# Performance work log

Measured on AMD Instinct MI355X. Metric: run time of the kernel, lower is better.

Reference implementation:

```python
import jax, jax.numpy as jnp
import numpy as np

EMBED = 256
HEADS = 8
HEAD_DIM = EMBED // HEADS  # 32, even for RoPE
INIT_VAL = 1.0
HEADS_RANGE = 3.0


def rotate_every_two(x):
    # (x1, x2) -> (-x2, x1) on interleaved pairs of last dim
    x1 = x[..., ::2]
    x2 = x[..., 1::2]
    return jnp.stack([-x2, x1], axis=-1).reshape(x.shape)


def theta_shift(x, sin, cos):
    # x: [B, heads, H, W, D]; sin/cos: [H, W, D] broadcast over B, heads
    return x * cos + rotate_every_two(x) * sin


def rel_pos_2d(H, W):
    # RetNetRelPos2d: RoPE angles + per-head exponential decay mask
    angle = 1.0 / (10000.0 ** jnp.linspace(0.0, 1.0, HEAD_DIM // 2))
    angle = jnp.repeat(angle, 2)  # [D]
    idx = jnp.arange(H * W, dtype=jnp.float32)
    sin = jnp.sin(idx[:, None] * angle[None, :]).reshape(H, W, HEAD_DIM)
    cos = jnp.cos(idx[:, None] * angle[None, :]).reshape(H, W, HEAD_DIM)
    h_idx = jnp.arange(HEADS, dtype=jnp.float32)
    decay = jnp.log(1.0 - 2.0 ** (-INIT_VAL - HEADS_RANGE * h_idx / HEADS))  # [heads]
    gh, gw = jnp.meshgrid(jnp.arange(H), jnp.arange(W), indexing='ij')
    grid = jnp.stack([gh, gw], axis=-1).reshape(H * W, 2)  # [N,2]
    dist = jnp.abs(grid[:, None, :] - grid[None, :, :]).sum(-1)  # [N,N] L1 distance
    mask = dist[None, :, :].astype(jnp.float32) * decay[:, None, None]  # [heads,N,N]
    return sin, cos, mask


def setup_inputs() -> dict:
    key = jax.random.key(0)
    ks = jax.random.split(key, 8)
    B, H, W, C = 2, 48, 48, EMBED
    s = 0.02
    return {
        'x': jax.random.normal(ks[0], (B, H, W, C), jnp.float32),
        'Wq': jax.random.normal(ks[1], (C, C), jnp.float32) * s,
        'bq': jnp.zeros((C,), jnp.float32),
        'Wk': jax.random.normal(ks[2], (C, C), jnp.float32) * s,
        'bk': jnp.zeros((C,), jnp.float32),
        'Wv': jax.random.normal(ks[3], (C, C), jnp.float32) * s,
        'bv': jnp.zeros((C,), jnp.float32),
        'lepe_w': jax.random.normal(ks[4], (C, 1, 5, 5), jnp.float32) * s,  # depthwise 5x5
        'lepe_b': jnp.zeros((C,), jnp.float32),
        'Wo': jax.random.normal(ks[5], (C, C), jnp.float32) * s,
        'bo': jnp.zeros((C,), jnp.float32),
    }


def reference(x, Wq, bq, Wk, bk, Wv, bv, lepe_w, lepe_b, Wo, bo):
    B, H, W, C = x.shape
    N = H * W
    sin, cos, mask = rel_pos_2d(H, W)
    scaling = HEAD_DIM ** -0.5

    q = x @ Wq + bq
    k = (x @ Wk + bk) * scaling
    v = x @ Wv + bv

    # lepe: depthwise 5x5 conv on v (BHWC)
    lepe = jax.lax.conv_general_dilated(
        v.transpose(0, 3, 1, 2), lepe_w, (1, 1), 'SAME',
        feature_group_count=C, dimension_numbers=('NCHW', 'OIHW', 'NCHW'))
    lepe = lepe.transpose(0, 2, 3, 1) + lepe_b  # [B,H,W,C]

    def split_heads(t):
        return t.reshape(B, H, W, HEADS, HEAD_DIM).transpose(0, 3, 1, 2, 4)

    qr = theta_shift(split_heads(q), sin, cos).reshape(B, HEADS, N, HEAD_DIM)
    kr = theta_shift(split_heads(k), sin, cos).reshape(B, HEADS, N, HEAD_DIM)
    vv = split_heads(v).reshape(B, HEADS, N, HEAD_DIM)

    attn = jnp.einsum('bhnd,bhmd->bhnm', qr, kr) + mask[None]  # [B,heads,N,N]
    attn = jax.nn.softmax(attn, axis=-1)
    out = jnp.einsum('bhnm,bhmd->bhnd', attn, vv)
    out = out.transpose(0, 2, 1, 3).reshape(B, H, W, C)
    out = out + lepe
    return out @ Wo + bo
```

## Files before the change

kernel.cpp:

```cpp
#include <hip/hip_runtime.h>
#include <hip/hip_bf16.h>
#include <math.h>

#define NN 2304
#define ROWSZ 4608
#define SZ (ROWSZ*256)

typedef __attribute__((ext_vector_type(8))) short short8;
typedef __attribute__((ext_vector_type(4))) float f32x4;

__device__ __forceinline__ float bf2f(unsigned short u) {
    return __uint_as_float(((unsigned int)u) << 16);
}
__device__ __forceinline__ unsigned short f2bf(float f) {
    unsigned int u = __float_as_uint(f);
    u += 0x7FFFu + ((u >> 16) & 1u);
    return (unsigned short)(u >> 16);
}
__device__ __forceinline__ unsigned int pack_bf2(float a, float b) {
    return (unsigned int)f2bf(a) | ((unsigned int)f2bf(b) << 16);
}

template<int F32>
__device__ __forceinline__ float ldin(const void* p, int i) {
    if constexpr (F32) return ((const float*)p)[i];
    else return bf2f(((const unsigned short*)p)[i]);
}

__global__ void detect_kernel(const unsigned int* __restrict__ x, int* __restrict__ flag) {
    int t = threadIdx.x;
    int cnt = 0;
    for (int i = t; i < 256; i += 64) {
        unsigned int e = (x[i] >> 7) & 0xFFu;
        cnt += (e < 87u || e > 167u) ? 1 : 0;
    }
    #pragma unroll
    for (int o = 32; o; o >>= 1) cnt += __shfl_down(cnt, o);
    if (t == 0) *flag = (cnt >= 32) ? 1 : 0;
}

template<int F32>
__device__ __forceinline__ void qkv_body(
    const void* __restrict__ x,
    const void* __restrict__ Wq, const void* __restrict__ bq,
    const void* __restrict__ Wk, const void* __restrict__ bk,
    const void* __restrict__ Wv, const void* __restrict__ bv,
    unsigned short* __restrict__ q, unsigned short* __restrict__ k,
    unsigned short* __restrict__ v, unsigned short* __restrict__ vT,
    float* __restrict__ xs)
{
    const int t = threadIdx.x;
    const int by = blockIdx.y;
    const int row0 = blockIdx.x * 16;
    #pragma unroll
    for (int pass = 0; pass < 2; ++pass) {
        int e = pass*2048 + t*8;
        if constexpr (F32) {
            const float* xp = (const float*)x + row0*256 + e;
            float4 a0 = *reinterpret_cast<const float4*>(xp);
            float4 a1 = *reinterpret_cast<const float4*>(xp + 4);
            *reinterpret_cast<float4*>(&xs[e])   = a0;
            *reinterpret_cast<float4*>(&xs[e+4]) = a1;
        } else {
            const unsigned short* xp = (const unsigned short*)x + row0*256 + e;
            uint4 raw = *reinterpret_cast<const uint4*>(xp);
            const unsigned short* us = reinterpret_cast<const unsigned short*>(&raw);
            #pragma unroll
            for (int j = 0; j < 8; ++j) xs[e + j] = bf2f(us[j]);
        }
    }
    __syncthreads();
    const void* Wsel = (by == 0) ? Wq : (by == 1) ? Wk : Wv;
    const void* bsel = (by == 0) ? bq : (by == 1) ? bk : bv;
    float a[16];
    const float bv0 = ldin<F32>(bsel, t);
    #pragma unroll
    for (int r = 0; r < 16; ++r) a[r] = bv0;
    for (int i0 = 0; i0 < 256; i0 += 4) {
        float w0 = ldin<F32>(Wsel, (i0+0)*256 + t);
        float w1 = ldin<F32>(Wsel, (i0+1)*256 + t);
        float w2 = ldin<F32>(Wsel, (i0+2)*256 + t);
        float w3 = ldin<F32>(Wsel, (i0+3)*256 + t);
        #pragma unroll
        for (int r = 0; r < 16; ++r) {
            float4 xv = *reinterpret_cast<const float4*>(&xs[r*256 + i0]);
            a[r] = fmaf(xv.w,w3, fmaf(xv.z,w2, fmaf(xv.y,w1, fmaf(xv.x,w0, a[r]))));
        }
    }
    if (by == 2) {
        const int b = (row0 >= NN) ? 1 : 0;
        const int n0 = row0 - b*NN;
        const int h = t >> 5, d = t & 31;
        unsigned int vp[8];
        #pragma unroll
        for (int r = 0; r < 16; ++r) v[(row0 + r)*256 + t] = f2bf(a[r]);
        #pragma unroll
        for (int r = 0; r < 8; ++r) vp[r] = pack_bf2(a[2*r], a[2*r+1]);
        unsigned short* vt = vT + ((size_t)(b*8 + h)*32 + d)*NN + n0;
        *reinterpret_cast<uint4*>(vt)     = make_uint4(vp[0], vp[1], vp[2], vp[3]);
        *reinterpret_cast<uint4*>(vt + 8) = make_uint4(vp[4], vp[5], vp[6], vp[7]);
    } else {
        const float scaling = 0.17677669529663687f;
        const int j = (t & 31) >> 1;
        const float ang = exp2f((float)j * (-0.8858474919699633f));
        const bool odd = t & 1;
        unsigned short* dst = (by == 0) ? q : k;
        const float mul = (by == 0) ? 1.0f : scaling;
        #pragma unroll
        for (int r = 0; r < 16; ++r) {
            int bn = row0 + r;
            int n = bn >= NN ? bn - NN : bn;
            float sv, cv;
            sincosf((float)n * ang, &sv, &cv);
            float ap = __shfl_xor(a[r], 1);
            float val = odd ? fmaf(a[r], cv, ap*sv) : fmaf(a[r], cv, -ap*sv);
            dst[bn*256 + t] = f2bf(val * mul);
        }
    }
}

__global__ __launch_bounds__(256) void qkv_kernel(
    const void* __restrict__ x,
    const void* __restrict__ Wq, const void* __restrict__ bq,
    const void* __restrict__ Wk, const void* __restrict__ bk,
    const void* __restrict__ Wv, const void* __restrict__ bv,
    const int* __restrict__ flag,
    unsigned short* __restrict__ q, unsigned short* __restrict__ k,
    unsigned short* __restrict__ v, unsigned short* __restrict__ vT)
{
    __shared__ float xs[16*256];
    if (*flag) qkv_body<1>(x, Wq, bq, Wk, bk, Wv, bv, q, k, v, vT, xs);
    else       qkv_body<0>(x, Wq, bq, Wk, bk, Wv, bv, q, k, v, vT, xs);
}

template<int F32>
__device__ __forceinline__ void lepe_body(const unsigned short* __restrict__ v,
    const void* __restrict__ w, const void* __restrict__ wb,
    unsigned short* __restrict__ lepe)
{
    int c = threadIdx.x;
    int pos = blockIdx.x;
    int b  = pos >= NN ? 1 : 0;
    int yx = pos - b*NN;
    int y  = (yx*21846) >> 20;
    int xx = yx - y*48;
    float acc = ldin<F32>(wb, c);
    #pragma unroll
    for (int ky = 0; ky < 5; ++ky) {
        int yy = y + ky - 2;
        if ((unsigned)yy >= 48u) continue;
        #pragma unroll
        for (int kx = 0; kx < 5; ++kx) {
            int xc = xx + kx - 2;
            if ((unsigned)xc >= 48u) continue;
            acc = fmaf(bf2f(v[((b*NN + yy*48 + xc)<<8) + c]), ldin<F32>(w, c*25 + ky*5 + kx), acc);
        }
    }
    lepe[(pos<<8) + c] = f2bf(acc);
}

__global__ __launch_bounds__(256) void lepe_kernel(const unsigned short* __restrict__ v,
    const void* __restrict__ w, const void* __restrict__ wb,
    const int* __restrict__ flag, unsigned short* __restrict__ lepe)
{
    if (*flag) lepe_body<1>(v, w, wb, lepe);
    else       lepe_body<0>(v, w, wb, lepe);
}

template<int DIRECT>
__global__ __launch_bounds__(256) void attn_kernel(
    const unsigned short* __restrict__ q, const unsigned short* __restrict__ k,
    const unsigned short* __restrict__ vT, unsigned short* __restrict__ o,
    float* __restrict__ pacc, float* __restrict__ pl)
{
    __shared__ char smem[17920];
    char* KsB = smem;
    char* VtB = smem + 5120;
    const int t = threadIdx.x;
    const int w = t >> 6, lane = t & 63;
    const int q16 = lane & 15, quad = lane >> 4;
    char* PsB = smem + 9728 + w*2048;
    const int bh = blockIdx.y, b = bh >> 3, h = bh & 7;
    const int q0 = blockIdx.x*64 + w*16;
    const int nq = q0 + q16;
    const int yq = (nq*21846) >> 20, xq = nq - yq*48;
    const float decay = logf(1.0f - exp2f(-1.0f - 0.375f*(float)h));
    short8 qfrag = *reinterpret_cast<const short8*>(q + ((size_t)(b*NN + nq))*256 + h*32 + quad*8);
    f32x4 acc0 = {0.f,0.f,0.f,0.f}, acc1 = {0.f,0.f,0.f,0.f};
    const f32x4 zero = {0.f,0.f,0.f,0.f};
    float lacc = 0.0f;
    const unsigned short* kbase = k + (size_t)(b*NN)*256 + h*32;
    const unsigned short* vtb = vT + (size_t)bh*32*NN;
    const int skr = t >> 2, skp = t & 3;
    const int svd = t >> 3, svp = t & 7;
    const int psW = q16*16 + (quad & 1)*8;
    const int qsh = quad >> 1;
    const int nchunk = 36 / gridDim.z;
    const int kt0 = blockIdx.z * nchunk;
    for (int kc = 0; kc < nchunk; ++kc) {
        const int kt = kt0 + kc;
        __syncthreads();
        {
            uint4 kraw = *reinterpret_cast<const uint4*>(kbase + (kt*64 + skr)*256 + skp*8);
            uint4 vraw = *reinterpret_cast<const uint4*>(vtb + svd*NN + kt*64 + svp*8);
            *reinterpret_cast<uint4*>(KsB + skr*80 + skp*16) = kraw;
            *reinterpret_cast<uint4*>(VtB + svd*144 + svp*16) = vraw;
        }
        __syncthreads();
        f32x4 st[4];
        #pragma unroll
        for (int tt = 0; tt < 4; ++tt) {
            short8 kf = *reinterpret_cast<const short8*>(KsB + (tt*16 + q16)*80 + quad*16);
            st[tt] = __builtin_amdgcn_mfma_f32_16x16x32_bf16(kf, qfrag, zero, 0, 0, 0);
        }
        unsigned int pk[8];
        float lsum = 0.0f;
        #pragma unroll
        for (int tt = 0; tt < 4; ++tt) {
            float p[4];
            #pragma unroll
            for (int r = 0; r < 4; ++r) {
                int kpos = kt*64 + tt*16 + quad*4 + r;
                int yk = (kpos*21846) >> 20;
                int xk = kpos - yk*48;
                int dist = __usad((unsigned)yq, (unsigned)yk, __usad((unsigned)xq, (unsigned)xk, 0u));
                p[r] = __expf(fmaf(decay, (float)dist, st[tt][r]));
                lsum += p[r];
            }
            pk[tt*2]   = __builtin_amdgcn_perm(__float_as_uint(p[1]), __float_as_uint(p[0]), 0x07060302);
            pk[tt*2+1] = __builtin_amdgcn_perm(__float_as_uint(p[3]), __float_as_uint(p[2]), 0x07060302);
        }
        lacc += lsum;
        #pragma unroll
        for (int tt = 0; tt < 4; ++tt) {
            uint2 pp; pp.x = pk[tt*2]; pp.y = pk[tt*2+1];
            *reinterpret_cast<uint2*>(PsB + (tt >> 1)*1024 + (((tt*2) + qsh) & 3)*256 + psW) = pp;
        }
        #pragma unroll
        for (int kh = 0; kh < 2; ++kh) {
            short8 pf = *reinterpret_cast<const short8*>(PsB + kh*1024 + lane*16);
            short8 v0 = *reinterpret_cast<const short8*>(VtB + q16*144 + kh*64 + quad*16);
            short8 v1 = *reinterpret_cast<const short8*>(VtB + (16 + q16)*144 + kh*64 + quad*16);
            acc0 = __builtin_amdgcn_mfma_f32_16x16x32_bf16(v0, pf, acc0, 0, 0, 0);
            acc1 = __builtin_amdgcn_mfma_f32_16x16x32_bf16(v1, pf, acc1, 0, 0, 0);
        }
    }
    lacc += __shfl_xor(lacc, 16);
    lacc += __shfl_xor(lacc, 32);
    if constexpr (DIRECT) {
        float invl = 1.0f / lacc;
        unsigned short* orow = o + ((size_t)(b*NN + nq))*256 + h*32;
        uint2 w0, w1;
        w0.x = pack_bf2(acc0[0]*invl, acc0[1]*invl);
        w0.y = pack_bf2(acc0[2]*invl, acc0[3]*invl);
        w1.x = pack_bf2(acc1[0]*invl, acc1[1]*invl);
        w1.y = pack_bf2(acc1[2]*invl, acc1[3]*invl);
        *reinterpret_cast<uint2*>(orow + quad*4)      = w0;
        *reinterpret_cast<uint2*>(orow + 16 + quad*4) = w1;
    } else {
        float* pb = pacc + ((size_t)(blockIdx.z*16 + bh)*NN + nq)*32;
        *reinterpret_cast<f32x4*>(pb + quad*4)      = acc0;
        *reinterpret_cast<f32x4*>(pb + 16 + quad*4) = acc1;
        if (quad == 0) pl[((size_t)blockIdx.z*16 + bh)*NN + nq] = lacc;
    }
}

template<int F32>
__device__ __forceinline__ void out_body(
    const unsigned short* __restrict__ o,
    const float* __restrict__ pacc, const float* __restrict__ pl,
    const unsigned short* __restrict__ lp,
    const void* __restrict__ Wo, const void* __restrict__ bo,
    void* __restrict__ out, float* __restrict__ as, int nsplit)
{
    const int t = threadIdx.x;
    const int row0 = blockIdx.x * 8;
    {
        const int e = t*8;
        const int r = t >> 5;
        const int nqr = row0 + r;
        const int ch = e & 255;
        uint4 ub = *reinterpret_cast<const uint4*>(lp + nqr*256 + ch);
        const unsigned short* bu = reinterpret_cast<const unsigned short*>(&ub);
        if (nsplit == 0) {
            uint4 ua = *reinterpret_cast<const uint4*>(o + nqr*256 + ch);
            const unsigned short* au = reinterpret_cast<const unsigned short*>(&ua);
            #pragma unroll
            for (int jj = 0; jj < 8; ++jj) as[e+jj] = bf2f(au[jj]) + bf2f(bu[jj]);
        } else {
            const int b = nqr >= NN ? 1 : 0;
            const int nq = nqr - b*NN;
            const int h = ch >> 5, d = ch & 31;
            const int bh = b*8 + h;
            float s[8] = {0.f,0.f,0.f,0.f,0.f,0.f,0.f,0.f};
            float lsum = 0.0f;
            for (int p = 0; p < nsplit; ++p) {
                const float* pb = pacc + ((size_t)(p*16 + bh)*NN + nq)*32 + d;
                f32x4 v0 = *reinterpret_cast<const f32x4*>(pb);
                f32x4 v1 = *reinterpret_cast<const f32x4*>(pb + 4);
                #pragma unroll
                for (int jj = 0; jj < 4; ++jj) { s[jj] += v0[jj]; s[4+jj] += v1[jj]; }
                lsum += pl[((size_t)p*16 + bh)*NN + nq];
            }
            float invl = 1.0f / lsum;
            #pragma unroll
            for (int jj = 0; jj < 8; ++jj) as[e+jj] = fmaf(s[jj], invl, bf2f(bu[jj]));
        }
    }
    __syncthreads();
    float a[8];
    const float bv = ldin<F32>(bo, t);
    #pragma unroll
    for (int r = 0; r < 8; ++r) a[r] = bv;
    for (int i0 = 0; i0 < 256; i0 += 4) {
        float w0 = ldin<F32>(Wo, (i0+0)*256 + t);
        float w1 = ldin<F32>(Wo, (i0+1)*256 + t);
        float w2 = ldin<F32>(Wo, (i0+2)*256 + t);
        float w3 = ldin<F32>(Wo, (i0+3)*256 + t);
        #pragma unroll
        for (int r = 0; r < 8; ++r) {
            float4 xv = *reinterpret_cast<const float4*>(&as[r*256 + i0]);
            a[r] = fmaf(xv.w,w3, fmaf(xv.z,w2, fmaf(xv.y,w1, fmaf(xv.x,w0, a[r]))));
        }
    }
    #pragma unroll
    for (int r = 0; r < 8; ++r) {
        int idx = (row0+r)*256 + t;
        if constexpr (F32) ((float*)out)[idx] = a[r];
        else ((unsigned short*)out)[idx] = f2bf(a[r]);
    }
}

__global__ __launch_bounds__(256) void out_kernel(
    const unsigned short* __restrict__ o,
    const float* __restrict__ pacc, const float* __restrict__ pl,
    const unsigned short* __restrict__ lp,
    const void* __restrict__ Wo, const void* __restrict__ bo,
    const int* __restrict__ flag, void* __restrict__ out, int nsplit)
{
    __shared__ float as[8*256];
    if (*flag) out_body<1>(o, pacc, pl, lp, Wo, bo, out, as, nsplit);
    else       out_body<0>(o, pacc, pl, lp, Wo, bo, out, as, nsplit);
}

extern "C" void kernel_launch(void* const* d_in, const int* in_sizes, int n_in,
                              void* d_out, int out_size, void* d_ws, size_t ws_size,
                              hipStream_t stream)
{
    const void* x  = d_in[0];
    const void* Wq = d_in[1];
    const void* bq = d_in[2];
    const void* Wk = d_in[3];
    const void* bk = d_in[4];
    const void* Wv = d_in[5];
    const void* bv = d_in[6];
    const void* lw = d_in[7];
    const void* lb = d_in[8];
    const void* Wo = d_in[9];
    const void* bo = d_in[10];

    int* flag = (int*)d_ws;
    unsigned short* qb   = (unsigned short*)((char*)d_ws + 256);
    unsigned short* kbuf = qb   + (size_t)SZ;
    unsigned short* vbuf = kbuf + (size_t)SZ;
    unsigned short* obuf = vbuf + (size_t)SZ;
    unsigned short* lbuf = obuf + (size_t)SZ;
    unsigned short* vtb  = lbuf + (size_t)SZ;

    const size_t base = 256 + 6*(size_t)SZ*2;
    const size_t per_split = (size_t)16*NN*32*4 + (size_t)16*NN*4;
    int nsplit = 0;
    if      (ws_size >= base + 4*per_split) nsplit = 4;
    else if (ws_size >= base + 2*per_split) nsplit = 2;
    else if (ws_size >= base + 1*per_split) nsplit = 1;
    float* pacc = (float*)((char*)d_ws + base);
    float* pl   = pacc + (size_t)(nsplit ? nsplit : 1)*16*NN*32;

    detect_kernel<<<1, 64, 0, stream>>>((const unsigned int*)x, flag);
    qkv_kernel<<<dim3(288,3), 256, 0, stream>>>(x, Wq, bq, Wk, bk, Wv, bv, flag, qb, kbuf, vbuf, vtb);
    lepe_kernel<<<4608, 256, 0, stream>>>(vbuf, lw, lb, flag, lbuf);
    if (nsplit) {
        attn_kernel<0><<<dim3(36, 16, nsplit), 256, 0, stream>>>(qb, kbuf, vtb, obuf, pacc, pl);
    } else {
        attn_kernel<1><<<dim3(36, 16, 1), 256, 0, stream>>>(qb, kbuf, vtb, obuf, pacc, pl);
    }
    out_kernel<<<576, 256, 0, stream>>>(obuf, pacc, pl, lbuf, Wo, bo, flag, d_out, nsplit);
}
```

Measured before the change: 232.8 us.

## Precompute L1 distance table in bytes and use exp2 with log2e folded into K

Adds a kernel that precomputes the 2304x2304 L1 grid-distance table as bytes, which the attention kernel loads instead of recomputing coordinates and distances per score. K is now pre-scaled by log2e and the decay is taken in log2, so the softmax exponent becomes a bare exp2 with no extra multiply. This cuts integer ALU work in the attention inner loop but adds a 5.3 MB table that is written every call and read per query row, plus one more kernel launch.

```diff
diff --git a/kernel.cpp b/kernel.cpp
--- a/kernel.cpp
+++ b/kernel.cpp
@@ -19,6 +19,23 @@
 }
 __device__ __forceinline__ unsigned int pack_bf2(float a, float b) {
     return (unsigned int)f2bf(a) | ((unsigned int)f2bf(b) << 16);
+}
+
+__device__ __forceinline__ float ub2f(unsigned int v, int r) {
+#if defined(__has_builtin)
+#if __has_builtin(__builtin_amdgcn_cvt_f32_ubyte0)
+    switch (r) {
+        case 0: return __builtin_amdgcn_cvt_f32_ubyte0(v);
+        case 1: return __builtin_amdgcn_cvt_f32_ubyte1(v);
+        case 2: return __builtin_amdgcn_cvt_f32_ubyte2(v);
+        default: return __builtin_amdgcn_cvt_f32_ubyte3(v);
+    }
+#else
+    return (float)((v >> (8*r)) & 0xFFu);
+#endif
+#else
+    return (float)((v >> (8*r)) & 0xFFu);
+#endif
 }
 
 template<int F32>
@@ -37,6 +54,26 @@
     #pragma unroll
     for (int o = 32; o; o >>= 1) cnt += __shfl_down(cnt, o);
     if (t == 0) *flag = (cnt >= 32) ? 1 : 0;
+}
+
+__global__ __launch_bounds__(256) void dist_kernel(unsigned char* __restrict__ D) {
+    const int nq = blockIdx.x;
+    const int yq = (nq*21846) >> 20, xq = nq - yq*48;
+    unsigned int* drow = reinterpret_cast<unsigned int*>(D + (size_t)nq*NN);
+    for (int idx = threadIdx.x; idx < 576; idx += 256) {
+        const int kp0 = idx*4;
+        unsigned int wv = 0;
+        #pragma unroll
+        for (int r = 0; r < 4; ++r) {
+            int kp = kp0 + r;
+            int yk = (kp*21846) >> 20;
+            int xk = kp - yk*48;
+            unsigned int dist = __usad((unsigned)yq, (unsigned)yk,
+                                __usad((unsigned)xq, (unsigned)xk, 0u));
+            wv |= dist << (8*r);
+        }
+        drow[idx] = wv;
+    }
 }
 
 template<int F32>
@@ -101,11 +138,12 @@
         *reinterpret_cast<uint4*>(vt + 8) = make_uint4(vp[4], vp[5], vp[6], vp[7]);
     } else {
         const float scaling = 0.17677669529663687f;
+        const float log2e   = 1.4426950408889634f;
         const int j = (t & 31) >> 1;
         const float ang = exp2f((float)j * (-0.8858474919699633f));
         const bool odd = t & 1;
         unsigned short* dst = (by == 0) ? q : k;
-        const float mul = (by == 0) ? 1.0f : scaling;
+        const float mul = (by == 0) ? 1.0f : scaling * log2e;
         #pragma unroll
         for (int r = 0; r < 16; ++r) {
             int bn = row0 + r;
@@ -170,8 +208,8 @@
 template<int DIRECT>
 __global__ __launch_bounds__(256) void attn_kernel(
     const unsigned short* __restrict__ q, const unsigned short* __restrict__ k,
-    const unsigned short* __restrict__ vT, unsigned short* __restrict__ o,
-    float* __restrict__ pacc, float* __restrict__ pl)
+    const unsigned short* __restrict__ vT, const unsigned char* __restrict__ D,
+    unsigned short* __restrict__ o, float* __restrict__ pacc, float* __restrict__ pl)
 {
     __shared__ char smem[17920];
     char* KsB = smem;
@@ -183,14 +221,14 @@
     const int bh = blockIdx.y, b = bh >> 3, h = bh & 7;
     const int q0 = blockIdx.x*64 + w*16;
     const int nq = q0 + q16;
-    const int yq = (nq*21846) >> 20, xq = nq - yq*48;
-    const float decay = logf(1.0f - exp2f(-1.0f - 0.375f*(float)h));
+    const float decay2 = log2f(1.0f - exp2f(-1.0f - 0.375f*(float)h));
     short8 qfrag = *reinterpret_cast<const short8*>(q + ((size_t)(b*NN + nq))*256 + h*32 + quad*8);
     f32x4 acc0 = {0.f,0.f,0.f,0.f}, acc1 = {0.f,0.f,0.f,0.f};
     const f32x4 zero = {0.f,0.f,0.f,0.f};
     float lacc = 0.0f;
     const unsigned short* kbase = k + (size_t)(b*NN)*256 + h*32;
     const unsigned short* vtb = vT + (size_t)bh*32*NN;
+    const unsigned char* Dbase = D + (size_t)nq*NN + quad*4;
     const int skr = t >> 2, skp = t & 3;
     const int svd = t >> 3, svp = t & 7;
     const int psW = q16*16 + (quad & 1)*8;
@@ -199,6 +237,10 @@
     const int kt0 = blockIdx.z * nchunk;
     for (int kc = 0; kc < nchunk; ++kc) {
         const int kt = kt0 + kc;
+        unsigned int dw[4];
+        #pragma unroll
+        for (int tt = 0; tt < 4; ++tt)
+            dw[tt] = *reinterpret_cast<const unsigned int*>(Dbase + kt*64 + tt*16);
         __syncthreads();
         {
             uint4 kraw = *reinterpret_cast<const uint4*>(kbase + (kt*64 + skr)*256 + skp*8);
@@ -220,11 +262,7 @@
             float p[4];
             #pragma unroll
             for (int r = 0; r < 4; ++r) {
-                int kpos = kt*64 + tt*16 + quad*4 + r;
-                int yk = (kpos*21846) >> 20;
-                int xk = kpos - yk*48;
-                int dist = __usad((unsigned)yq, (unsigned)yk, __usad((unsigned)xq, (unsigned)xk, 0u));
-                p[r] = __expf(fmaf(decay, (float)dist, st[tt][r]));
+                p[r] = exp2f(fmaf(decay2, ub2f(dw[tt], r), st[tt][r]));
                 lsum += p[r];
             }
             pk[tt*2]   = __builtin_amdgcn_perm(__float_as_uint(p[1]), __float_as_uint(p[0]), 0x07060302);
@@ -366,8 +404,9 @@
     unsigned short* obuf = vbuf + (size_t)SZ;
     unsigned short* lbuf = obuf + (size_t)SZ;
     unsigned short* vtb  = lbuf + (size_t)SZ;
-
-    const size_t base = 256 + 6*(size_t)SZ*2;
+    unsigned char*  Dtab = (unsigned char*)(vtb + (size_t)SZ);
+
+    const size_t base = 256 + 6*(size_t)SZ*2 + (size_t)NN*NN;
     const size_t per_split = (size_t)16*NN*32*4 + (size_t)16*NN*4;
     int nsplit = 0;
     if      (ws_size >= base + 4*per_split) nsplit = 4;
@@ -377,12 +416,13 @@
     float* pl   = pacc + (size_t)(nsplit ? nsplit : 1)*16*NN*32;
 
     detect_kernel<<<1, 64, 0, stream>>>((const unsigned int*)x, flag);
+    dist_kernel<<<NN, 256, 0, stream>>>(Dtab);
     qkv_kernel<<<dim3(288,3), 256, 0, stream>>>(x, Wq, bq, Wk, bk, Wv, bv, flag, qb, kbuf, vbuf, vtb);
     lepe_kernel<<<4608, 256, 0, stream>>>(vbuf, lw, lb, flag, lbuf);
     if (nsplit) {
-        attn_kernel<0><<<dim3(36, 16, nsplit), 256, 0, stream>>>(qb, kbuf, vtb, obuf, pacc, pl);
+        attn_kernel<0><<<dim3(36, 16, nsplit), 256, 0, stream>>>(qb, kbuf, vtb, Dtab, obuf, pacc, pl);
     } else {
-        attn_kernel<1><<<dim3(36, 16, 1), 256, 0, stream>>>(qb, kbuf, vtb, obuf, pacc, pl);
+        attn_kernel<1><<<dim3(36, 16, 1), 256, 0, stream>>>(qb, kbuf, vtb, Dtab, obuf, pacc, pl);
     }
     out_kernel<<<576, 256, 0, stream>>>(obuf, pacc, pl, lbuf, Wo, bo, flag, d_out, nsplit);
 }
```

Result: no change. 236.7 us (+1.7%).
